# Optimization experiments

Measured on AMD Instinct MI355X. Metric: run time of the kernel, lower is better.

## Reference

```python
import jax, jax.numpy as jnp
import numpy as np
import math

N_LAYERS, B, T, D, H, F, V = 4, 2, 1024, 1024, 16, 4096, 50257
HD = D // H
EPS = 1e-6  # flax LayerNorm default

def _slopes(n):
    # get_slopes for power-of-2 n (H=16)
    start = 2.0 ** (-2.0 ** (-(math.log2(n) - 3.0)))
    return np.array([start * (start ** i) for i in range(n)], dtype=np.float32)

SLOPES = jnp.asarray(_slopes(H))

def _ln(x, s, b):
    m = jnp.mean(x, axis=-1, keepdims=True)
    v = jnp.mean(jnp.square(x - m), axis=-1, keepdims=True)
    return (x - m) * jax.lax.rsqrt(v + EPS) * s + b

def setup_inputs():
    key = jax.random.key(0)
    ks = jax.random.split(key, 8)
    g = lambda k, shape: 0.02 * jax.random.normal(k, shape, jnp.float32)
    return {
        'tokens': jax.random.randint(ks[0], (B, T), 0, V, dtype=jnp.int32),
        'wte': g(ks[1], (V, D)),
        'ln1_s': jnp.ones((N_LAYERS, D), jnp.float32), 'ln1_b': jnp.zeros((N_LAYERS, D), jnp.float32),
        'Wq': g(ks[2], (N_LAYERS, D, D)), 'bq': jnp.zeros((N_LAYERS, D), jnp.float32),
        'Wk': g(ks[3], (N_LAYERS, D, D)), 'bk': jnp.zeros((N_LAYERS, D), jnp.float32),
        'Wv': g(ks[4], (N_LAYERS, D, D)), 'bv': jnp.zeros((N_LAYERS, D), jnp.float32),
        'Wo': g(ks[5], (N_LAYERS, D, D)), 'bo': jnp.zeros((N_LAYERS, D), jnp.float32),
        'ln2_s': jnp.ones((N_LAYERS, D), jnp.float32), 'ln2_b': jnp.zeros((N_LAYERS, D), jnp.float32),
        'Wfi': g(ks[6], (N_LAYERS, D, F)), 'bfi': jnp.zeros((N_LAYERS, F), jnp.float32),
        'Wfo': g(ks[7], (N_LAYERS, F, D)), 'bfo': jnp.zeros((N_LAYERS, D), jnp.float32),
        'lnf_s': jnp.ones((D,), jnp.float32), 'lnf_b': jnp.zeros((D,), jnp.float32),
    }

def _forward(tokens, wte, ln1_s, ln1_b, Wq, bq, Wk, bk, Wv, bv, Wo, bo, ln2_s, ln2_b, Wfi, bfi, Wfo, bfo, lnf_s, lnf_b):
    x = wte[tokens]  # [B, T, D] (no wpe when alibi_attn=True)
    # ALiBi bias, last-row variant from source: bias[h, j] = -slope[h] * (T-1-j), shared across queries
    alibi = (-SLOPES[:, None] * (T - 1 - jnp.arange(T, dtype=jnp.float32)))[None, :, None, :]  # [1,H,1,T]
    causal = jnp.tril(jnp.ones((T, T), dtype=bool))[None, None]  # [1,1,T,T]
    neg_inf = jnp.finfo(jnp.float32).min
    scale = 1.0 / math.sqrt(HD)
    for i in range(N_LAYERS):
        h = _ln(x, ln1_s[i], ln1_b[i])
        q = (h @ Wq[i] + bq[i]).reshape(B, T, H, HD)
        k = (h @ Wk[i] + bk[i]).reshape(B, T, H, HD)
        v = (h @ Wv[i] + bv[i]).reshape(B, T, H, HD)
        scores = jnp.einsum('bqhd,bkhd->bhqk', q, k) * scale + alibi
        scores = jnp.where(causal, scores, neg_inf)
        p = jax.nn.softmax(scores, axis=-1)
        attn = jnp.einsum('bhqk,bkhd->bqhd', p, v).reshape(B, T, D)
        x = x + attn @ Wo[i] + bo[i]
        h2 = _ln(x, ln2_s[i], ln2_b[i])
        x = x + jax.nn.gelu(h2 @ Wfi[i] + bfi[i]) @ Wfo[i] + bfo[i]
    out = _ln(x, lnf_s, lnf_b)
    return out @ wte.T  # tied-embedding logits [B, T, V]

def reference(tokens, wte, ln1_s, ln1_b, Wq, bq, Wk, bk, Wv, bv, Wo, bo, ln2_s, ln2_b, Wfi, bfi, Wfo, bfo, lnf_s, lnf_b):
    return _forward(tokens, wte, ln1_s, ln1_b, Wq, bq, Wk, bk, Wv, bv, Wo, bo, ln2_s, ln2_b, Wfi, bfi, Wfo, bfo, lnf_s, lnf_b)
```

## Files before the change

### kernel.cpp

```cpp
#include <hip/hip_runtime.h>
#include <hip/hip_bf16.h>


typedef unsigned short u16;
typedef unsigned int u32;
typedef __attribute__((ext_vector_type(8))) short bf16x8;
typedef __attribute__((ext_vector_type(4))) float f32x4;

#define DEVINL static __device__ __forceinline__

DEVINL u16 f2bf(float f){ __hip_bfloat16 h = __float2bfloat16(f); return *reinterpret_cast<u16*>(&h); }

DEVINL bf16x8 cvt8(float4 a, float4 b){
  bf16x8 r;
  r[0] = (short)f2bf(a.x); r[1] = (short)f2bf(a.y);
  r[2] = (short)f2bf(a.z); r[3] = (short)f2bf(a.w);
  r[4] = (short)f2bf(b.x); r[5] = (short)f2bf(b.y);
  r[6] = (short)f2bf(b.z); r[7] = (short)f2bf(b.w);
  return r;
}

DEVINL void gload16(const u16* g, u16* l){
  __builtin_amdgcn_global_load_lds((const __attribute__((address_space(1))) void*)g,
                                   (__attribute__((address_space(3))) void*)l, 16, 0, 0);
}

__global__ __launch_bounds__(256) void cvt_bf16_kernel(const float* __restrict__ src,
    u16* __restrict__ dst, int n8){
  int i = blockIdx.x*256 + threadIdx.x;
  if (i >= n8) return;
  const float4* p = (const float4*)(src + (size_t)i*8);
  float4 a = p[0], b = p[1];
  *(bf16x8*)(dst + (size_t)i*8) = cvt8(a, b);
}

__global__ __launch_bounds__(256) void embed_kernel(const int* __restrict__ tok,
    const float* __restrict__ wte, float* __restrict__ x){
  int m = blockIdx.x, t = threadIdx.x;
  int token = tok[m];
  float4 f = ((const float4*)(wte + (size_t)token*1024))[t];
  ((float4*)(x + (size_t)m*1024))[t] = f;
}

__global__ __launch_bounds__(256) void ln_kernel(const float* __restrict__ x,
    const float* __restrict__ gam, const float* __restrict__ bet, u16* __restrict__ out){
  int m = blockIdx.x, t = threadIdx.x;
  float4 v = ((const float4*)(x + (size_t)m*1024))[t];
  float s  = v.x + v.y + v.z + v.w;
  float s2 = v.x*v.x + v.y*v.y + v.z*v.z + v.w*v.w;
  #pragma unroll
  for (int o = 32; o > 0; o >>= 1){ s += __shfl_xor(s, o); s2 += __shfl_xor(s2, o); }
  __shared__ float red[8];
  int w = t >> 6;
  if ((t & 63) == 0){ red[w] = s; red[4 + w] = s2; }
  __syncthreads();
  s  = red[0] + red[1] + red[2] + red[3];
  s2 = red[4] + red[5] + red[6] + red[7];
  float mean = s * (1.0f/1024.0f);
  float var  = s2 * (1.0f/1024.0f) - mean*mean;
  float inv  = rsqrtf(var + 1e-6f);
  float4 gv = ((const float4*)gam)[t];
  float4 bv = ((const float4*)bet)[t];
  u32 o0 = f2bf((v.x - mean)*inv*gv.x + bv.x);
  u32 o1 = f2bf((v.y - mean)*inv*gv.y + bv.y);
  u32 o2 = f2bf((v.z - mean)*inv*gv.z + bv.z);
  u32 o3 = f2bf((v.w - mean)*inv*gv.w + bv.w);
  uint2 ov; ov.x = o0 | (o1 << 16); ov.y = o2 | (o3 << 16);
  ((uint2*)(out + (size_t)m*1024))[t] = ov;
}

template<typename T>
DEVINL void transpose_tile(const T* __restrict__ src, u16* __restrict__ dst,
                           int ss, int ds, int c0, int r0, int t){
  __shared__ alignas(16) u16 tile[64][68];
  #pragma unroll
  for (int e = 0; e < 4; ++e){
    int idx = (e << 8) + t;
    int r = idx >> 4, c = (idx & 15) << 2;
    if constexpr (sizeof(T) == 4){
      float4 f = *(const float4*)(src + (size_t)(r0 + r)*ss + c0 + c);
      tile[r][c+0] = f2bf(f.x); tile[r][c+1] = f2bf(f.y);
      tile[r][c+2] = f2bf(f.z); tile[r][c+3] = f2bf(f.w);
    } else {
      uint2 u = *(const uint2*)(src + (size_t)(r0 + r)*ss + c0 + c);
      tile[r][c+0] = (u16)(u.x & 0xffffu); tile[r][c+1] = (u16)(u.x >> 16);
      tile[r][c+2] = (u16)(u.y & 0xffffu); tile[r][c+3] = (u16)(u.y >> 16);
    }
  }
  __syncthreads();
  #pragma unroll
  for (int e = 0; e < 4; ++e){
    int idx = (e << 8) + t;
    int cc = idx >> 4, rr = (idx & 15) << 2;
    uint2 u;
    u.x = (u32)tile[rr+0][cc] | ((u32)tile[rr+1][cc] << 16);
    u.y = (u32)tile[rr+2][cc] | ((u32)tile[rr+3][cc] << 16);
    *(uint2*)(dst + (size_t)(c0 + cc)*ds + r0 + rr) = u;
  }
}

template<typename T>
__global__ __launch_bounds__(256) void transpose_kernel(const T* __restrict__ src,
    u16* __restrict__ dst, int ss, int ds){
  transpose_tile<T>(src, dst, ss, ds, blockIdx.x << 6, blockIdx.y << 6, threadIdx.x);
}

__global__ __launch_bounds__(256) void transpose3_kernel(const float* __restrict__ s0,
    const float* __restrict__ s1, const float* __restrict__ s2, u16* __restrict__ dst){
  const float* src = (blockIdx.z == 0) ? s0 : ((blockIdx.z == 1) ? s1 : s2);
  transpose_tile<float>(src, dst + (size_t)blockIdx.z*1048576, 1024, 1024,
                        blockIdx.x << 6, blockIdx.y << 6, threadIdx.x);
}

__global__ __launch_bounds__(256) void concat3_kernel(const float* __restrict__ a,
    const float* __restrict__ b, const float* __restrict__ c, float* __restrict__ o){
  int t = blockIdx.x*256 + threadIdx.x;
  o[t] = (t < 1024) ? a[t] : ((t < 2048) ? b[t - 1024] : c[t - 2048]);
}

template<bool BF32, int BN>
__global__ __launch_bounds__(256) void gemm_nt(const u16* __restrict__ A,
    const void* __restrict__ Bp, const float* __restrict__ bias,
    u16* __restrict__ Cb, float* __restrict__ Cf,
    int N, int K, int mode){
  constexpr int NI = BN / 32;
  constexpr int ASTR = 4096;
  constexpr int BSTR = BN*32;
  constexpr int SELEMS = 2*(ASTR + BSTR);
  __shared__ alignas(16) u16 S[SELEMS];
  const int tid = threadIdx.x, lane = tid & 63, w = tid >> 6;
  const int wr = w >> 1, wc = w & 1;
  const int nx = gridDim.x;
  const int nwg = nx << 4;
  const int flat = blockIdx.y * nx + blockIdx.x;
  const int qch = nwg >> 3, rch = nwg & 7;
  const int xcd = flat & 7, idxc = flat >> 3;
  const int nf = (xcd < rch ? xcd*(qch+1) : rch*(qch+1) + (xcd-rch)*qch) + idxc;
  const int m0 = (nf & 15) << 7;
  const int n0 = (nf >> 4) * BN;
  const int r = lane & 15, qq = lane >> 4;
  const int srow = (w << 4) + (lane >> 2);
  const int sus  = lane & 3;
  const f32x4 vzero = {0.f, 0.f, 0.f, 0.f};
  f32x4 acc[4][NI];
  #pragma unroll
  for (int i = 0; i < 4; ++i)
    #pragma unroll
    for (int j = 0; j < NI; ++j) acc[i][j] = vzero;

  const u16* pa0 = A + (size_t)(m0 + srow)*K + (sus << 3);
  const u16* pa1 = pa0 + (size_t)64*K;
  int nr0 = n0 + srow;      if (nr0 >= N) nr0 = N - 1;
  int nr1 = n0 + 64 + srow; if (nr1 >= N) nr1 = N - 1;
  const u16*   pbh0 = nullptr; const u16*   pbh1 = nullptr;
  const float* pbf0 = nullptr; const float* pbf1 = nullptr;
  if constexpr (BF32){
    pbf0 = (const float*)Bp + (size_t)nr0*K + (sus << 3);
    pbf1 = (const float*)Bp + (size_t)nr1*K + (sus << 3);
  } else {
    pbh0 = (const u16*)Bp + (size_t)nr0*K + (sus << 3);
    pbh1 = (const u16*)Bp + (size_t)nr1*K + (sus << 3);
  }

  const int nkt = K >> 5;
  const int sw0 = (srow << 5) + (sus << 3);
  const int sw1 = ((srow + 64) << 5) + (sus << 3);

  {
    u16* Ab = S; u16* Bb = S + ASTR;
    gload16(pa0, &Ab[w << 9]);
    gload16(pa1, &Ab[2048 + (w << 9)]);
    if constexpr (BF32){
      float4 g0 = *(const float4*)pbf0, g1 = *(const float4*)(pbf0 + 4);
      float4 g2 = *(const float4*)pbf1, g3 = *(const float4*)(pbf1 + 4);
      *(bf16x8*)&Bb[sw0] = cvt8(g0, g1);
      *(bf16x8*)&Bb[sw1] = cvt8(g2, g3);
    } else {
      gload16(pbh0, &Bb[w << 9]);
      if constexpr (BN == 128) gload16(pbh1, &Bb[2048 + (w << 9)]);
    }
    __syncthreads();
  }

  int buf = 0;
  for (int kt = 0; kt < nkt; ++kt){
    u16* Ab = S + buf*(ASTR + BSTR);
    u16* Bb = Ab + ASTR;
    const int nb = buf ^ 1;
    u16* An = S + nb*(ASTR + BSTR);
    u16* Bn = An + ASTR;
    float4 g0, g1, g2, g3;
    const bool more = (kt + 1 < nkt);
    if (more){
      const int k1 = (kt + 1) << 5;
      gload16(pa0 + k1, &An[w << 9]);
      gload16(pa1 + k1, &An[2048 + (w << 9)]);
      if constexpr (BF32){
        g0 = *(const float4*)(pbf0 + k1); g1 = *(const float4*)(pbf0 + k1 + 4);
        g2 = *(const float4*)(pbf1 + k1); g3 = *(const float4*)(pbf1 + k1 + 4);
      } else {
        gload16(pbh0 + k1, &Bn[w << 9]);
        if constexpr (BN == 128) gload16(pbh1 + k1, &Bn[2048 + (w << 9)]);
      }
    }
    bf16x8 af[4], bfv[NI];
    #pragma unroll
    for (int mi = 0; mi < 4; ++mi){
      int rowi = (wr << 6) + (mi << 4) + r;
      af[mi] = *(const bf16x8*)&Ab[(rowi << 5) + (qq << 3)];
    }
    #pragma unroll
    for (int ni = 0; ni < NI; ++ni){
      int rowi = wc*(BN/2) + (ni << 4) + r;
      bfv[ni] = *(const bf16x8*)&Bb[(rowi << 5) + (qq << 3)];
    }
    #pragma unroll
    for (int mi = 0; mi < 4; ++mi)
      #pragma unroll
      for (int ni = 0; ni < NI; ++ni)
        acc[mi][ni] = __builtin_amdgcn_mfma_f32_16x16x32_bf16(af[mi], bfv[ni], acc[mi][ni], 0, 0, 0);
    if constexpr (BF32){
      if (more){
        *(bf16x8*)&Bn[sw0] = cvt8(g0, g1);
        *(bf16x8*)&Bn[sw1] = cvt8(g2, g3);
      }
    }
    __syncthreads();
    buf = nb;
  }

  if constexpr (BN == 128){
    if (mode == 3){
      float* ep = (float*)S;
      const int row16 = tid >> 3;
      const int wr2 = row16 >> 4, rr = row16 & 15;
      const int q8 = tid & 7;
      #pragma unroll
      for (int c = 0; c < 4; ++c){
        __syncthreads();
        #pragma unroll
        for (int ni = 0; ni < NI; ++ni)
          #pragma unroll
          for (int rg = 0; rg < 4; ++rg)
            ep[wr*2112 + ((qq << 2) + rg)*132 + wc*64 + (ni << 4) + r] = acc[c][ni][rg];
        __syncthreads();
        const float* src = &ep[wr2*2112 + rr*132];
        const int grow = m0 + wr2*64 + (c << 4) + rr;
        const size_t basef = (size_t)grow*N + n0;
        const int al = (int)((16 - (basef & 15)) & 15);
        if (q8 < 7){
          const int c0 = al + (q8 << 4);
          float* dst = &Cf[basef + c0];
          if (n0 + c0 + 15 < N){
            #pragma unroll
            for (int qk = 0; qk < 4; ++qk){
              float4 v;
              v.x = src[c0 + qk*4 + 0]; v.y = src[c0 + qk*4 + 1];
              v.z = src[c0 + qk*4 + 2]; v.w = src[c0 + qk*4 + 3];
              *(float4*)(dst + qk*4) = v;
            }
          } else {
            for (int i = 0; i < 16; ++i)
              if (n0 + c0 + i < N) dst[i] = src[c0 + i];
          }
        } else {
          for (int i = 0; i < al; ++i)
            if (n0 + i < N) Cf[basef + i] = src[i];
          for (int i = al + 112; i < 128; ++i)
            if (n0 + i < N) Cf[basef + i] = src[i];
        }
      }
      return;
    }
  }

  #pragma unroll
  for (int ni = 0; ni < NI; ++ni){
    int col = n0 + wc*(BN/2) + (ni << 4) + r;
    if (col >= N) continue;
    float bb = bias ? bias[col] : 0.0f;
    #pragma unroll
    for (int mi = 0; mi < 4; ++mi){
      #pragma unroll
      for (int rg = 0; rg < 4; ++rg){
        int rowg = m0 + (wr << 6) + (mi << 4) + (qq << 2) + rg;
        float v = acc[mi][ni][rg] + bb;
        if (mode == 1){
          float z = 1.5957691216057308f * (v + 0.044715f*v*v*v);
          v = v - v / (__expf(z) + 1.0f);
        }
        if (mode == 2){
          Cf[(size_t)rowg*N + col] += v;
        } else {
          Cb[(size_t)rowg*N + col] = f2bf(v);
        }
      }
    }
  }
}

__global__ __launch_bounds__(256) void attn_kernel(const u16* __restrict__ qkv,
    const u16* __restrict__ vt, u16* __restrict__ o){
  const int qt = blockIdx.x;
  const int bh = blockIdx.y;
  const int b = bh >> 4, h = bh & 15;
  const int tid = threadIdx.x, lane = tid & 63, w = tid >> 6;
  const int r = lane & 15, qq = lane >> 4;
  const int qrow0 = (qt << 6) + (w << 4);

  __shared__ alignas(16) u16 Ks[64*72];
  __shared__ alignas(16) u16 Vs[64*72];
  __shared__ alignas(16) u16 Ps[4][16*72];

  const u16* qp = qkv + (size_t)(b*1024 + qrow0 + r)*3072 + h*64 + (qq << 3);
  bf16x8 qf0 = *(const bf16x8*)qp;
  bf16x8 qf1 = *(const bf16x8*)(qp + 32);

  const f32x4 vzero = {0.f, 0.f, 0.f, 0.f};
  float m_run[4], l_run[4];
  f32x4 acc_o[4];
  #pragma unroll
  for (int i = 0; i < 4; ++i){ m_run[i] = -1e30f; l_run[i] = 0.0f; acc_o[i] = vzero; }
  const float slope = exp2f(-0.5f*(float)(h + 1));

  for (int jt = 0; jt <= qt; ++jt){
    const int kv0 = jt << 6;
    __syncthreads();
    #pragma unroll
    for (int e = 0; e < 2; ++e){
      int idx = (e << 8) + tid;
      int row = idx >> 3, ch = idx & 7;
      *(bf16x8*)&Ks[row*72 + (ch << 3)] =
        *(const bf16x8*)(qkv + (size_t)(b*1024 + kv0 + row)*3072 + 1024 + h*64 + (ch << 3));
      *(bf16x8*)&Vs[row*72 + (ch << 3)] =
        *(const bf16x8*)(vt + (size_t)(h*64 + row)*2048 + b*1024 + kv0 + (ch << 3));
    }
    __syncthreads();

    f32x4 sa[4];
    #pragma unroll
    for (int ni = 0; ni < 4; ++ni){
      f32x4 z = vzero;
      bf16x8 kf0 = *(const bf16x8*)&Ks[(ni*16 + r)*72 + (qq << 3)];
      bf16x8 kf1 = *(const bf16x8*)&Ks[(ni*16 + r)*72 + 32 + (qq << 3)];
      z = __builtin_amdgcn_mfma_f32_16x16x32_bf16(qf0, kf0, z, 0, 0, 0);
      z = __builtin_amdgcn_mfma_f32_16x16x32_bf16(qf1, kf1, z, 0, 0, 0);
      sa[ni] = z;
    }
    float mx[4] = {-1e30f, -1e30f, -1e30f, -1e30f};
    #pragma unroll
    for (int ni = 0; ni < 4; ++ni){
      int colg = kv0 + ni*16 + r;
      float ab = -slope * (float)(1023 - colg);
      #pragma unroll
      for (int rg = 0; rg < 4; ++rg){
        int rowg = (qt << 6) + (w << 4) + (qq << 2) + rg;
        float sv = sa[ni][rg]*0.125f + ab;
        sv = fminf(sv, 60.0f);
        sv = (colg > rowg) ? -1e30f : sv;
        sa[ni][rg] = sv;
        mx[rg] = fmaxf(mx[rg], sv);
      }
    }
    #pragma unroll
    for (int off = 1; off < 16; off <<= 1){
      #pragma unroll
      for (int rg = 0; rg < 4; ++rg) mx[rg] = fmaxf(mx[rg], __shfl_xor(mx[rg], off));
    }
    float alpha[4], rs[4];
    #pragma unroll
    for (int rg = 0; rg < 4; ++rg){
      float mn = fmaxf(m_run[rg], mx[rg]);
      alpha[rg] = __expf(m_run[rg] - mn);
      m_run[rg] = mn;
      rs[rg] = 0.0f;
    }
    u16* pw = &Ps[w][0];
    #pragma unroll
    for (int ni = 0; ni < 4; ++ni){
      #pragma unroll
      for (int rg = 0; rg < 4; ++rg){
        float p = __expf(sa[ni][rg] - m_run[rg]);
        rs[rg] += p;
        pw[(qq*4 + rg)*72 + ni*16 + r] = f2bf(p);
      }
    }
    #pragma unroll
    for (int off = 1; off < 16; off <<= 1){
      #pragma unroll
      for (int rg = 0; rg < 4; ++rg) rs[rg] += __shfl_xor(rs[rg], off);
    }
    #pragma unroll
    for (int rg = 0; rg < 4; ++rg) l_run[rg] = l_run[rg]*alpha[rg] + rs[rg];
    #pragma unroll
    for (int ni = 0; ni < 4; ++ni)
      #pragma unroll
      for (int rg = 0; rg < 4; ++rg) acc_o[ni][rg] *= alpha[rg];
    __syncthreads();
    #pragma unroll
    for (int kk = 0; kk < 2; ++kk){
      bf16x8 pa = *(const bf16x8*)&pw[r*72 + (kk << 5) + (qq << 3)];
      #pragma unroll
      for (int ni = 0; ni < 4; ++ni){
        bf16x8 vf = *(const bf16x8*)&Vs[(ni*16 + r)*72 + (kk << 5) + (qq << 3)];
        acc_o[ni] = __builtin_amdgcn_mfma_f32_16x16x32_bf16(pa, vf, acc_o[ni], 0, 0, 0);
      }
    }
  }
  #pragma unroll
  for (int ni = 0; ni < 4; ++ni){
    #pragma unroll
    for (int rg = 0; rg < 4; ++rg){
      int rowg = b*1024 + (qt << 6) + (w << 4) + (qq << 2) + rg;
      o[(size_t)rowg*1024 + h*64 + ni*16 + r] = f2bf(acc_o[ni][rg] / l_run[rg]);
    }
  }
}

extern "C" void kernel_launch(void* const* d_in, const int* in_sizes, int n_in,
                              void* d_out, int out_size, void* d_ws, size_t ws_size,
                              hipStream_t stream){
  (void)in_sizes; (void)n_in; (void)out_size;
  const int*   tok  = (const int*)d_in[0];
  const float* wte  = (const float*)d_in[1];
  const float* ln1s = (const float*)d_in[2];
  const float* ln1b = (const float*)d_in[3];
  const float* Wq   = (const float*)d_in[4];
  const float* bq   = (const float*)d_in[5];
  const float* Wk   = (const float*)d_in[6];
  const float* bk   = (const float*)d_in[7];
  const float* Wv   = (const float*)d_in[8];
  const float* bv   = (const float*)d_in[9];
  const float* Wo   = (const float*)d_in[10];
  const float* bo   = (const float*)d_in[11];
  const float* ln2s = (const float*)d_in[12];
  const float* ln2b = (const float*)d_in[13];
  const float* Wfi  = (const float*)d_in[14];
  const float* bfi  = (const float*)d_in[15];
  const float* Wfo  = (const float*)d_in[16];
  const float* bfo  = (const float*)d_in[17];
  const float* lnfs = (const float*)d_in[18];
  const float* lnfb = (const float*)d_in[19];

  char* ws = (char*)d_ws;
  float* x   = (float*)(ws);
  u16* h     = (u16*)(ws + ( 8u << 20));
  u16* qkv   = (u16*)(ws + (12u << 20));
  u16* v_t   = (u16*)(ws + (24u << 20));
  u16* attnb = (u16*)(ws + (28u << 20));
  u16* ffn   = (u16*)(ws + (32u << 20));
  u16* wT    = (u16*)(ws + (48u << 20));
  float* b3  = (float*)(ws + (56u << 20));
  u16* wteb  = (u16*)(ws + (57u << 20));

  const size_t wteb_bytes = (size_t)50257 * 1024 * 2;
  const bool big_ws = ws_size >= ((size_t)(57u) << 20) + wteb_bytes;

  if (big_ws){
    cvt_bf16_kernel<<<25129, 256, 0, stream>>>(wte, wteb, 6432896);
  }
  embed_kernel<<<2048, 256, 0, stream>>>(tok, wte, x);
  for (int i = 0; i < 4; ++i){
    ln_kernel<<<2048, 256, 0, stream>>>(x, ln1s + i*1024, ln1b + i*1024, h);
    transpose3_kernel<<<dim3(16,16,3), 256, 0, stream>>>(
        Wq + (size_t)i*1048576, Wk + (size_t)i*1048576, Wv + (size_t)i*1048576, wT);
    concat3_kernel<<<12, 256, 0, stream>>>(bq + i*1024, bk + i*1024, bv + i*1024, b3);
    gemm_nt<false,128><<<dim3(24,16), 256, 0, stream>>>(h, wT, b3, qkv, nullptr, 3072, 1024, 0);
    transpose_kernel<u16><<<dim3(16,32), 256, 0, stream>>>(qkv + 2048, v_t, 3072, 2048);
    attn_kernel<<<dim3(16,32), 256, 0, stream>>>(qkv, v_t, attnb);
    transpose_kernel<float><<<dim3(16,16), 256, 0, stream>>>(Wo + (size_t)i*1048576, wT, 1024, 1024);
    gemm_nt<false,64><<<dim3(16,16), 256, 0, stream>>>(attnb, wT, bo + i*1024, nullptr, x, 1024, 1024, 2);
    ln_kernel<<<2048, 256, 0, stream>>>(x, ln2s + i*1024, ln2b + i*1024, h);
    transpose_kernel<float><<<dim3(64,16), 256, 0, stream>>>(Wfi + (size_t)i*4194304, wT, 4096, 1024);
    gemm_nt<false,128><<<dim3(32,16), 256, 0, stream>>>(h, wT, bfi + i*4096, ffn, nullptr, 4096, 1024, 1);
    transpose_kernel<float><<<dim3(16,64), 256, 0, stream>>>(Wfo + (size_t)i*4194304, wT, 1024, 4096);
    gemm_nt<false,64><<<dim3(16,16), 256, 0, stream>>>(ffn, wT, bfo + i*1024, nullptr, x, 1024, 4096, 2);
  }
  ln_kernel<<<2048, 256, 0, stream>>>(x, lnfs, lnfb, h);
  if (big_ws){
    gemm_nt<false,128><<<dim3(393,16), 256, 0, stream>>>(h, wteb, nullptr, nullptr, (float*)d_out, 50257, 1024, 3);
  } else {
    gemm_nt<true,128><<<dim3(393,16), 256, 0, stream>>>(h, wte, nullptr, nullptr, (float*)d_out, 50257, 1024, 3);
  }
}
```

Measured before the change: 1.293 ms.

## Triple-buffer bf16 GEMM loads with vmcnt waits, swizzle LDS, nontemporal logits stores

For the bf16-B GEMM path, the two-stage LDS double buffer becomes a three-stage ring. Loads are issued two k-tiles ahead and synchronised with explicit s_waitcnt vmcnt plus raw s_barrier instead of a full __syncthreads, so global latency hides behind more MFMA work. An XOR swizzle on the LDS column chunk is added to cut bank conflicts on fragment reads. The fp32 logits epilogue now uses nontemporal stores to avoid polluting the cache with the large output. The extra buffer raises LDS use per block, which may lower occupancy, and the hand-counted vmcnt values must match the number of issued loads.

```diff
diff --git a/kernel.cpp b/kernel.cpp
--- a/kernel.cpp
+++ b/kernel.cpp
@@ -8,6 +8,7 @@
 typedef __attribute__((ext_vector_type(4))) float f32x4;
 
 #define DEVINL static __device__ __forceinline__
+#define WAITVM(N) asm volatile("s_waitcnt vmcnt(" #N ")" ::: "memory")
 
 DEVINL u16 f2bf(float f){ __hip_bfloat16 h = __float2bfloat16(f); return *reinterpret_cast<u16*>(&h); }
 
@@ -126,8 +127,9 @@
   constexpr int NI = BN / 32;
   constexpr int ASTR = 4096;
   constexpr int BSTR = BN*32;
-  constexpr int SELEMS = 2*(ASTR + BSTR);
-  __shared__ alignas(16) u16 S[SELEMS];
+  constexpr int BUFSZ = ASTR + BSTR;
+  constexpr int NBUF = BF32 ? 2 : 3;
+  __shared__ alignas(16) u16 S[NBUF*BUFSZ];
   const int tid = threadIdx.x, lane = tid & 63, w = tid >> 6;
   const int wr = w >> 1, wc = w & 1;
   const int nx = gridDim.x;
@@ -141,6 +143,8 @@
   const int r = lane & 15, qq = lane >> 4;
   const int srow = (w << 4) + (lane >> 2);
   const int sus  = lane & 3;
+  const int su2  = sus ^ ((lane >> 3) & 3);
+  const int rsw  = (r >> 1) & 3;
   const f32x4 vzero = {0.f, 0.f, 0.f, 0.f};
   f32x4 acc[4][NI];
   #pragma unroll
@@ -148,7 +152,7 @@
     #pragma unroll
     for (int j = 0; j < NI; ++j) acc[i][j] = vzero;
 
-  const u16* pa0 = A + (size_t)(m0 + srow)*K + (sus << 3);
+  const u16* pa0 = A + (size_t)(m0 + srow)*K + (su2 << 3);
   const u16* pa1 = pa0 + (size_t)64*K;
   int nr0 = n0 + srow;      if (nr0 >= N) nr0 = N - 1;
   int nr1 = n0 + 64 + srow; if (nr1 >= N) nr1 = N - 1;
@@ -158,76 +162,113 @@
     pbf0 = (const float*)Bp + (size_t)nr0*K + (sus << 3);
     pbf1 = (const float*)Bp + (size_t)nr1*K + (sus << 3);
   } else {
-    pbh0 = (const u16*)Bp + (size_t)nr0*K + (sus << 3);
-    pbh1 = (const u16*)Bp + (size_t)nr1*K + (sus << 3);
+    pbh0 = (const u16*)Bp + (size_t)nr0*K + (su2 << 3);
+    pbh1 = (const u16*)Bp + (size_t)nr1*K + (su2 << 3);
   }
 
   const int nkt = K >> 5;
-  const int sw0 = (srow << 5) + (sus << 3);
-  const int sw1 = ((srow + 64) << 5) + (sus << 3);
-
-  {
-    u16* Ab = S; u16* Bb = S + ASTR;
-    gload16(pa0, &Ab[w << 9]);
-    gload16(pa1, &Ab[2048 + (w << 9)]);
-    if constexpr (BF32){
+
+#define GEMM_STAGE(dst, kofs) do {                                        \
+    gload16(pa0 + (kofs), &(dst)[w << 9]);                                \
+    gload16(pa1 + (kofs), &(dst)[2048 + (w << 9)]);                       \
+    gload16(pbh0 + (kofs), &(dst)[ASTR + (w << 9)]);                      \
+    if constexpr (BN == 128)                                              \
+      gload16(pbh1 + (kofs), &(dst)[ASTR + 2048 + (w << 9)]);             \
+  } while(0)
+
+  if constexpr (!BF32){
+    u16 *rd = S, *nxt = S + BUFSZ, *st = S + 2*BUFSZ;
+    GEMM_STAGE(rd, 0);
+    GEMM_STAGE(nxt, 32);
+    if constexpr (BN == 128) { WAITVM(4); } else { WAITVM(3); }
+    __builtin_amdgcn_sched_barrier(0);
+    __builtin_amdgcn_s_barrier();
+    __builtin_amdgcn_sched_barrier(0);
+    for (int kt = 0; kt < nkt; ++kt){
+      const bool more2 = (kt + 2 < nkt);
+      if (more2){ GEMM_STAGE(st, (kt + 2) << 5); }
+      bf16x8 af[4], bfv[NI];
+      #pragma unroll
+      for (int mi = 0; mi < 4; ++mi){
+        int rowi = (wr << 6) + (mi << 4) + r;
+        af[mi] = *(const bf16x8*)&rd[(rowi << 5) + ((qq ^ rsw) << 3)];
+      }
+      #pragma unroll
+      for (int ni = 0; ni < NI; ++ni){
+        int rowi = wc*(BN/2) + (ni << 4) + r;
+        bfv[ni] = *(const bf16x8*)&rd[ASTR + (rowi << 5) + ((qq ^ rsw) << 3)];
+      }
+      #pragma unroll
+      for (int mi = 0; mi < 4; ++mi)
+        #pragma unroll
+        for (int ni = 0; ni < NI; ++ni)
+          acc[mi][ni] = __builtin_amdgcn_mfma_f32_16x16x32_bf16(af[mi], bfv[ni], acc[mi][ni], 0, 0, 0);
+      if (kt + 1 < nkt){
+        if (more2){
+          if constexpr (BN == 128) { WAITVM(4); } else { WAITVM(3); }
+        } else {
+          WAITVM(0);
+        }
+        __builtin_amdgcn_sched_barrier(0);
+        __builtin_amdgcn_s_barrier();
+        __builtin_amdgcn_sched_barrier(0);
+        u16* t0 = rd; rd = nxt; nxt = st; st = t0;
+      }
+    }
+  } else {
+    const int sw0 = (srow << 5) + (sus << 3);
+    const int sw1 = ((srow + 64) << 5) + (sus << 3);
+    {
+      u16* Ab = S; u16* Bb = S + ASTR;
+      gload16(pa0, &Ab[w << 9]);
+      gload16(pa1, &Ab[2048 + (w << 9)]);
       float4 g0 = *(const float4*)pbf0, g1 = *(const float4*)(pbf0 + 4);
       float4 g2 = *(const float4*)pbf1, g3 = *(const float4*)(pbf1 + 4);
       *(bf16x8*)&Bb[sw0] = cvt8(g0, g1);
       *(bf16x8*)&Bb[sw1] = cvt8(g2, g3);
-    } else {
-      gload16(pbh0, &Bb[w << 9]);
-      if constexpr (BN == 128) gload16(pbh1, &Bb[2048 + (w << 9)]);
-    }
-    __syncthreads();
-  }
-
-  int buf = 0;
-  for (int kt = 0; kt < nkt; ++kt){
-    u16* Ab = S + buf*(ASTR + BSTR);
-    u16* Bb = Ab + ASTR;
-    const int nb = buf ^ 1;
-    u16* An = S + nb*(ASTR + BSTR);
-    u16* Bn = An + ASTR;
-    float4 g0, g1, g2, g3;
-    const bool more = (kt + 1 < nkt);
-    if (more){
-      const int k1 = (kt + 1) << 5;
-      gload16(pa0 + k1, &An[w << 9]);
-      gload16(pa1 + k1, &An[2048 + (w << 9)]);
-      if constexpr (BF32){
+      __syncthreads();
+    }
+    int buf = 0;
+    for (int kt = 0; kt < nkt; ++kt){
+      u16* Ab = S + buf*BUFSZ;
+      u16* Bb = Ab + ASTR;
+      const int nb = buf ^ 1;
+      u16* An = S + nb*BUFSZ;
+      u16* Bn = An + ASTR;
+      float4 g0, g1, g2, g3;
+      const bool more = (kt + 1 < nkt);
+      if (more){
+        const int k1 = (kt + 1) << 5;
+        gload16(pa0 + k1, &An[w << 9]);
+        gload16(pa1 + k1, &An[2048 + (w << 9)]);
         g0 = *(const float4*)(pbf0 + k1); g1 = *(const float4*)(pbf0 + k1 + 4);
         g2 = *(const float4*)(pbf1 + k1); g3 = *(const float4*)(pbf1 + k1 + 4);
-      } else {
-        gload16(pbh0 + k1, &Bn[w << 9]);
-        if constexpr (BN == 128) gload16(pbh1 + k1, &Bn[2048 + (w << 9)]);
-      }
-    }
-    bf16x8 af[4], bfv[NI];
-    #pragma unroll
-    for (int mi = 0; mi < 4; ++mi){
-      int rowi = (wr << 6) + (mi << 4) + r;
-      af[mi] = *(const bf16x8*)&Ab[(rowi << 5) + (qq << 3)];
-    }
-    #pragma unroll
-    for (int ni = 0; ni < NI; ++ni){
-      int rowi = wc*(BN/2) + (ni << 4) + r;
-      bfv[ni] = *(const bf16x8*)&Bb[(rowi << 5) + (qq << 3)];
-    }
-    #pragma unroll
-    for (int mi = 0; mi < 4; ++mi)
-      #pragma unroll
-      for (int ni = 0; ni < NI; ++ni)
-        acc[mi][ni] = __builtin_amdgcn_mfma_f32_16x16x32_bf16(af[mi], bfv[ni], acc[mi][ni], 0, 0, 0);
-    if constexpr (BF32){
+      }
+      bf16x8 af[4], bfv[NI];
+      #pragma unroll
+      for (int mi = 0; mi < 4; ++mi){
+        int rowi = (wr << 6) + (mi << 4) + r;
+        af[mi] = *(const bf16x8*)&Ab[(rowi << 5) + ((qq ^ rsw) << 3)];
+      }
+      #pragma unroll
+      for (int ni = 0; ni < NI; ++ni){
+        int rowi = wc*(BN/2) + (ni << 4) + r;
+        bfv[ni] = *(const bf16x8*)&Bb[(rowi << 5) + (qq << 3)];
+      }
+      #pragma unroll
+      for (int mi = 0; mi < 4; ++mi)
+        #pragma unroll
+        for (int ni = 0; ni < NI; ++ni)
+          acc[mi][ni] = __builtin_amdgcn_mfma_f32_16x16x32_bf16(af[mi], bfv[ni], acc[mi][ni], 0, 0, 0);
       if (more){
         *(bf16x8*)&Bn[sw0] = cvt8(g0, g1);
         *(bf16x8*)&Bn[sw1] = cvt8(g2, g3);
       }
-    }
-    __syncthreads();
-    buf = nb;
-  }
+      __syncthreads();
+      buf = nb;
+    }
+  }
+#undef GEMM_STAGE
 
   if constexpr (BN == 128){
     if (mode == 3){
@@ -254,10 +295,10 @@
           if (n0 + c0 + 15 < N){
             #pragma unroll
             for (int qk = 0; qk < 4; ++qk){
-              float4 v;
-              v.x = src[c0 + qk*4 + 0]; v.y = src[c0 + qk*4 + 1];
-              v.z = src[c0 + qk*4 + 2]; v.w = src[c0 + qk*4 + 3];
-              *(float4*)(dst + qk*4) = v;
+              f32x4 v;
+              v[0] = src[c0 + qk*4 + 0]; v[1] = src[c0 + qk*4 + 1];
+              v[2] = src[c0 + qk*4 + 2]; v[3] = src[c0 + qk*4 + 3];
+              __builtin_nontemporal_store(v, (f32x4*)(dst + qk*4));
             }
           } else {
             for (int i = 0; i < 16; ++i)
```

Measured after the change: 1.529 ms. 18.2% more time.
